# Kernel tuning notes

Hardware: AMD Instinct MI355X
Metric: run time of the kernel (lower is better)

## Reference

```python
import jax, jax.numpy as jnp
import numpy as np

D_MODEL = 1024
NUM_HEADS = 16
D_K = D_MODEL // NUM_HEADS
B, S = 4, 2048
NEG_INF = -1.0e9  # matches torch masked_fill value


def setup_inputs() -> dict:
    key = jax.random.key(0)
    ks = jax.random.split(key, 6)
    scale = 1.0 / np.sqrt(D_MODEL)
    x = jax.random.normal(ks[0], (B, S, D_MODEL), dtype=jnp.float32)
    # causal mask, broadcast over batch and heads: [1,1,S,S]
    mask = jnp.tril(jnp.ones((S, S), dtype=jnp.int32))[None, None]
    Wq = jax.random.normal(ks[1], (D_MODEL, D_MODEL), dtype=jnp.float32) * scale
    Wk = jax.random.normal(ks[2], (D_MODEL, D_MODEL), dtype=jnp.float32) * scale
    Wv = jax.random.normal(ks[3], (D_MODEL, D_MODEL), dtype=jnp.float32) * scale
    Wo = jax.random.normal(ks[4], (D_MODEL, D_MODEL), dtype=jnp.float32) * scale
    bq = jnp.zeros((D_MODEL,), jnp.float32)
    bk = jnp.zeros((D_MODEL,), jnp.float32)
    bv = jnp.zeros((D_MODEL,), jnp.float32)
    bo = jnp.zeros((D_MODEL,), jnp.float32)
    return {"x": x, "mask": mask, "Wq": Wq, "bq": bq, "Wk": Wk, "bk": bk,
            "Wv": Wv, "bv": bv, "Wo": Wo, "bo": bo}


def reference(x, mask, Wq, bq, Wk, bk, Wv, bv, Wo, bo):
    b, s, d = x.shape
    # projections (torch Linear: y = x @ W.T + b)
    q = (x @ Wq.T + bq).reshape(b, s, NUM_HEADS, D_K).transpose(0, 2, 1, 3)  # [B,H,S,Dk]
    k = (x @ Wk.T + bk).reshape(b, s, NUM_HEADS, D_K).transpose(0, 2, 1, 3)
    v = (x @ Wv.T + bv).reshape(b, s, NUM_HEADS, D_K).transpose(0, 2, 1, 3)
    scores = jnp.einsum("bhqd,bhkd->bhqk", q, k) / jnp.sqrt(jnp.float32(D_K))
    scores = jnp.where(mask == 0, NEG_INF, scores)
    attn = jax.nn.softmax(scores, axis=-1)
    out = jnp.einsum("bhqk,bhkd->bhqd", attn, v)  # [B,H,S,Dk]
    out = out.transpose(0, 2, 1, 3).reshape(b, s, d)
    return out @ Wo.T + bo
```

## Files before the change

### kernel.cpp

```cpp
#include <hip/hip_runtime.h>
#include <hip/hip_bf16.h>

#define D_MODEL 1024
#define NUM_HEADS 16
#define DK 64
#define BATCH 4
#define SEQ 2048

typedef __hip_bfloat16 bf16;
typedef __attribute__((ext_vector_type(8))) short bf16x8;
typedef __attribute__((ext_vector_type(4))) short bf16x4;
typedef __attribute__((ext_vector_type(4))) float f32x4;

typedef __attribute__((address_space(1))) const unsigned int gu32;
typedef __attribute__((address_space(3))) unsigned int lu32;

#define QSCALE (0.125f * 1.44269504089f)

__device__ __forceinline__ void gll16(const bf16* g, bf16* l) {
    __builtin_amdgcn_global_load_lds((gu32*)g, (lu32*)l, 16, 0, 0);
}

__device__ __forceinline__ bf16x8 frag_ld(const bf16* lds, int row, int h, int quad) {
    return *(const bf16x8*)(lds + row * 64 + (((h << 2) + quad) ^ (row & 7)) * 8);
}

__global__ __launch_bounds__(256)
void cvt_bf16(const float* __restrict__ x,  const float* __restrict__ Wq,
              const float* __restrict__ Wk, const float* __restrict__ Wv,
              const float* __restrict__ Wo, bf16* __restrict__ xb,
              bf16* __restrict__ Wb)
{
    size_t v = (size_t)blockIdx.x * 256 + threadIdx.x;
    size_t e = v * 4;
    const float* src; bf16* dst; size_t off;
    if (e < 8388608) { src = x; dst = xb; off = e; }
    else {
        size_t r = e - 8388608;
        int w = (int)(r >> 20);
        off = r & 1048575;
        src = (w == 0) ? Wq : (w == 1) ? Wk : (w == 2) ? Wv : Wo;
        dst = Wb + ((size_t)w << 20);
    }
    float4 f = *(const float4*)(src + off);
    bf16 o[4] = {__float2bfloat16(f.x), __float2bfloat16(f.y),
                 __float2bfloat16(f.z), __float2bfloat16(f.w)};
    *(bf16x4*)(dst + off) = *(const bf16x4*)o;
}

template<int MODE>
__global__ __launch_bounds__(512, 2)
void gemm_pipe(const bf16* __restrict__ A, const bf16* __restrict__ W,
               const float* __restrict__ bqv, const float* __restrict__ bkv,
               const float* __restrict__ bvv,
               bf16* __restrict__ Q, bf16* __restrict__ Kt, bf16* __restrict__ Vtr,
               float* __restrict__ fout)
{
    __shared__ bf16 lds[65536];

    const int t = threadIdx.x;
    const int wave = t >> 6, lane = t & 63;
    const int quad = lane >> 4, l16 = lane & 15;
    const int wm = wave >> 2, wn = wave & 3;

    int proj, colb;
    if (MODE == 0) { proj = blockIdx.x >> 2; colb = blockIdx.x & 3; }
    else           { proj = 3;               colb = blockIdx.x;     }
    const int rowBase = blockIdx.y * 256;

    const bf16* Ablk = A + (size_t)rowBase * 1024;
    const bf16* Bblk = W + ((size_t)proj << 20) + (size_t)colb * 256 * 1024;

    auto stage_tile = [&](int d, int k0) {
        bf16* Ad = lds + d * 16384;
        bf16* Bd = lds + 32768 + d * 16384;
        #pragma unroll
        for (int h = 0; h < 2; ++h)
            #pragma unroll
            for (int p = 0; p < 2; ++p) {
                int idx = t + p * 512;
                int row = idx >> 3, cl = idx & 7, cg = cl ^ (row & 7);
                gll16(Ablk + (size_t)(h * 128 + row) * 1024 + k0 + cg * 8,
                      Ad + h * 8192 + idx * 8);
                gll16(Bblk + (size_t)(h * 128 + row) * 1024 + k0 + cg * 8,
                      Bd + h * 8192 + idx * 8);
            }
    };

    f32x4 acc[8][4];
    #pragma unroll
    for (int mf = 0; mf < 8; ++mf)
        #pragma unroll
        for (int nf = 0; nf < 4; ++nf) acc[mf][nf] = (f32x4){0.f, 0.f, 0.f, 0.f};

    auto compute_tile = [&](int d) {
        const bf16* As = lds + d * 16384 + wm * 8192;
        const bf16* Bs = lds + 32768 + d * 16384 + (wn >> 1) * 8192;
        const int brow = (wn & 1) * 64;
        bf16x8 bfr[4][2];
        #pragma unroll
        for (int nf = 0; nf < 4; ++nf) {
            bfr[nf][0] = frag_ld(Bs, brow + nf * 16 + l16, 0, quad);
            bfr[nf][1] = frag_ld(Bs, brow + nf * 16 + l16, 1, quad);
        }
        __builtin_amdgcn_s_setprio(1);
        #pragma unroll
        for (int mf = 0; mf < 8; ++mf) {
            bf16x8 af0 = frag_ld(As, mf * 16 + l16, 0, quad);
            bf16x8 af1 = frag_ld(As, mf * 16 + l16, 1, quad);
            #pragma unroll
            for (int nf = 0; nf < 4; ++nf) {
                acc[mf][nf] = __builtin_amdgcn_mfma_f32_16x16x32_bf16(af0, bfr[nf][0], acc[mf][nf], 0, 0, 0);
                acc[mf][nf] = __builtin_amdgcn_mfma_f32_16x16x32_bf16(af1, bfr[nf][1], acc[mf][nf], 0, 0, 0);
            }
        }
        __builtin_amdgcn_s_setprio(0);
    };

    stage_tile(0, 0);
    stage_tile(1, 64);
    asm volatile("s_waitcnt vmcnt(8)" ::: "memory");
    __builtin_amdgcn_s_barrier();
    asm volatile("" ::: "memory");
    __builtin_amdgcn_sched_barrier(0);

    for (int kt = 0; kt < 16; ++kt) {
        const int d = kt & 1;
        compute_tile(d);

        asm volatile("s_waitcnt lgkmcnt(0)" ::: "memory");
        __builtin_amdgcn_sched_barrier(0);
        __builtin_amdgcn_s_barrier();
        asm volatile("" ::: "memory");

        if (kt + 2 < 16) {
            stage_tile(d, (kt + 2) * 64);
            asm volatile("s_waitcnt vmcnt(8)" ::: "memory");
        } else if (kt + 1 < 16) {
            asm volatile("s_waitcnt vmcnt(0)" ::: "memory");
        }
        if (kt + 1 < 16) {
            __builtin_amdgcn_s_barrier();
            asm volatile("" ::: "memory");
            __builtin_amdgcn_sched_barrier(0);
        }
    }

    if (MODE == 0) {
        const float* bias = proj == 0 ? bqv : (proj == 1 ? bkv : bvv);
        float bias4[4];
        #pragma unroll
        for (int nf = 0; nf < 4; ++nf)
            bias4[nf] = bias[colb * 256 + wn * 64 + nf * 16 + l16];
        const float oscale = proj == 0 ? QSCALE : 1.0f;
        #pragma unroll
        for (int mf = 0; mf < 8; ++mf)
            #pragma unroll
            for (int rr = 0; rr < 4; ++rr) {
                int r = rowBase + wm * 128 + mf * 16 + quad * 4 + rr;
                int b_ = r >> 11, s_ = r & 2047;
                #pragma unroll
                for (int nf = 0; nf < 4; ++nf) {
                    int c = colb * 256 + wn * 64 + nf * 16 + l16;
                    float v = (acc[mf][nf][rr] + bias4[nf]) * oscale;
                    int h_ = c >> 6, d_ = c & 63;
                    size_t bh = (size_t)(b_ * NUM_HEADS + h_);
                    if (proj == 2)
                        Vtr[(bh * DK + d_) * SEQ + s_] = __float2bfloat16(v);
                    else {
                        bf16* dst = proj == 0 ? Q : Kt;
                        dst[(bh * SEQ + s_) * DK + d_] = __float2bfloat16(v);
                    }
                }
            }
    } else {
        #pragma unroll
        for (int mf = 0; mf < 8; ++mf)
            #pragma unroll
            for (int rr = 0; rr < 4; ++rr) {
                int r = rowBase + wm * 128 + mf * 16 + quad * 4 + rr;
                #pragma unroll
                for (int nf = 0; nf < 4; ++nf) {
                    int c = colb * 256 + wn * 64 + nf * 16 + l16;
                    fout[(size_t)r * 1024 + c] = acc[mf][nf][rr] + bqv[c];
                }
            }
    }
}

#define AS 72

__device__ __forceinline__ void stage_attn(const bf16* __restrict__ Kb,
                                           const bf16* __restrict__ Vb,
                                           int k0, bf16* ks, bf16* vs, int t)
{
    #pragma unroll
    for (int p = 0; p < 2; ++p) {
        int idx = t + p * 256;
        int row = idx >> 3, cl = idx & 7;
        int cg = cl ^ (row & 7);
        gll16(Kb + (size_t)(k0 + row) * DK + cg * 8, ks + idx * 8);
        gll16(Vb + (size_t)row * SEQ + k0 + cg * 8, vs + idx * 8);
    }
}

__global__ __launch_bounds__(256)
void attn_mfma(const bf16* __restrict__ Q, const bf16* __restrict__ K,
               const bf16* __restrict__ Vt, bf16* __restrict__ ctx)
{
    __shared__ bf16 Ks[2][64 * 64];
    __shared__ bf16 Vs[2][64 * 64];
    __shared__ bf16 Ps[4][2][16 * AS];

    const int t    = threadIdx.x;
    const int wave = t >> 6, lane = t & 63;
    const int quad = lane >> 4, l16 = lane & 15;
    const int bh   = blockIdx.x;
    const int qbi  = 15 - blockIdx.y;
    const int b_ = bh >> 4, h_ = bh & 15;

    const bf16* Qb = Q  + (size_t)bh * SEQ * DK;
    const bf16* Kb = K  + (size_t)bh * SEQ * DK;
    const bf16* Vb = Vt + (size_t)bh * DK * SEQ;

    const int qb  = qbi * 128;
    const int ntiles = 2 * qbi + 2;

    bf16x8 qf[2][2];
    #pragma unroll
    for (int i = 0; i < 2; ++i) {
        const int qrow = qb + wave * 32 + i * 16 + l16;
        qf[i][0] = *(const bf16x8*)(Qb + (size_t)qrow * DK + quad * 8);
        qf[i][1] = *(const bf16x8*)(Qb + (size_t)qrow * DK + 32 + quad * 8);
    }

    f32x4 O[2][4];
    float lsum[2][4];
    #pragma unroll
    for (int i = 0; i < 2; ++i)
        #pragma unroll
        for (int nc = 0; nc < 4; ++nc) {
            O[i][nc] = (f32x4){0.f, 0.f, 0.f, 0.f};
            lsum[i][nc] = 0.f;
        }

    stage_attn(Kb, Vb, 0, Ks[0], Vs[0], t);
    __syncthreads();

    for (int kt = 0; kt < ntiles; ++kt) {
        const int cur = kt & 1;
        const int k0  = kt * 64;
        if (kt + 1 < ntiles)
            stage_attn(Kb, Vb, k0 + 64, Ks[cur ^ 1], Vs[cur ^ 1], t);

        const bool diag = (kt + 2 >= ntiles);
        const bool skip = (kt == ntiles - 1) && (wave < 2);

        if (!skip) {
            bf16x8 kf[4][2];
            #pragma unroll
            for (int h = 0; h < 4; ++h) {
                kf[h][0] = frag_ld(Ks[cur], h * 16 + l16, 0, quad);
                kf[h][1] = frag_ld(Ks[cur], h * 16 + l16, 1, quad);
            }

            #pragma unroll
            for (int i = 0; i < 2; ++i) {
                const int qrow0i = qb + wave * 32 + i * 16;
                float lacc[4];
                #pragma unroll
                for (int r = 0; r < 4; ++r) lacc[r] = lsum[i][r];
                #pragma unroll
                for (int h = 0; h < 4; ++h) {
                    f32x4 a = (f32x4){0.f, 0.f, 0.f, 0.f};
                    a = __builtin_amdgcn_mfma_f32_16x16x32_bf16(qf[i][0], kf[h][0], a, 0, 0, 0);
                    a = __builtin_amdgcn_mfma_f32_16x16x32_bf16(qf[i][1], kf[h][1], a, 0, 0, 0);
                    #pragma unroll
                    for (int r = 0; r < 4; ++r) {
                        float ss = a[r];
                        if (diag && (k0 + h * 16 + l16 > qrow0i + quad * 4 + r))
                            ss = -1e30f;
                        float p = exp2f(ss);
                        lacc[r] += p;
                        Ps[wave][i][(quad * 4 + r) * AS + h * 16 + l16] =
                            __float2bfloat16(p);
                    }
                }
                #pragma unroll
                for (int r = 0; r < 4; ++r) lsum[i][r] = lacc[r];
            }

            bf16x8 pf[2][2];
            #pragma unroll
            for (int i = 0; i < 2; ++i) {
                pf[i][0] = *(const bf16x8*)(&Ps[wave][i][l16 * AS + quad * 8]);
                pf[i][1] = *(const bf16x8*)(&Ps[wave][i][l16 * AS + 32 + quad * 8]);
            }
            __builtin_amdgcn_s_setprio(1);
            #pragma unroll
            for (int nc = 0; nc < 4; ++nc) {
                bf16x8 vf0 = frag_ld(Vs[cur], nc * 16 + l16, 0, quad);
                bf16x8 vf1 = frag_ld(Vs[cur], nc * 16 + l16, 1, quad);
                #pragma unroll
                for (int i = 0; i < 2; ++i) {
                    O[i][nc] = __builtin_amdgcn_mfma_f32_16x16x32_bf16(pf[i][0], vf0, O[i][nc], 0, 0, 0);
                    O[i][nc] = __builtin_amdgcn_mfma_f32_16x16x32_bf16(pf[i][1], vf1, O[i][nc], 0, 0, 0);
                }
            }
            __builtin_amdgcn_s_setprio(0);
        }
        __syncthreads();
    }

    #pragma unroll
    for (int i = 0; i < 2; ++i) {
        #pragma unroll
        for (int r = 0; r < 4; ++r) {
            #pragma unroll
            for (int off = 1; off < 16; off <<= 1)
                lsum[i][r] += __shfl_xor(lsum[i][r], off, 64);
        }
        #pragma unroll
        for (int nc = 0; nc < 4; ++nc)
            #pragma unroll
            for (int r = 0; r < 4; ++r) {
                const int row = qb + wave * 32 + i * 16 + quad * 4 + r;
                float v = O[i][nc][r] / lsum[i][r];
                ctx[((size_t)(b_ * SEQ + row)) * D_MODEL + h_ * DK + nc * 16 + l16] =
                    __float2bfloat16(v);
            }
    }
}

extern "C" void kernel_launch(void* const* d_in, const int* in_sizes, int n_in,
                              void* d_out, int out_size, void* d_ws, size_t ws_size,
                              hipStream_t stream) {
    const float* x  = (const float*)d_in[0];
    const float* Wq = (const float*)d_in[2];
    const float* bq = (const float*)d_in[3];
    const float* Wk = (const float*)d_in[4];
    const float* bk = (const float*)d_in[5];
    const float* Wv = (const float*)d_in[6];
    const float* bv = (const float*)d_in[7];
    const float* Wo = (const float*)d_in[8];
    const float* bo = (const float*)d_in[9];
    float* out = (float*)d_out;

    const size_t per = (size_t)BATCH * NUM_HEADS * SEQ * DK;
    bf16* Q   = (bf16*)d_ws;
    bf16* Kt  = Q  + per;
    bf16* Vtr = Kt + per;
    bf16* xb  = Vtr + per;
    bf16* ctx = xb;
    bf16* Wb  = xb + per;

    hipLaunchKernelGGL(cvt_bf16, dim3(12288), dim3(256), 0, stream,
                       x, Wq, Wk, Wv, Wo, xb, Wb);

    hipLaunchKernelGGL((gemm_pipe<0>), dim3(12, 32), dim3(512), 0, stream,
                       xb, Wb, bq, bk, bv, Q, Kt, Vtr, (float*)nullptr);

    hipLaunchKernelGGL(attn_mfma, dim3(64, 16), dim3(256), 0,
                       stream, Q, Kt, Vtr, ctx);

    hipLaunchKernelGGL((gemm_pipe<1>), dim3(4, 32), dim3(512), 0, stream,
                       ctx, Wb, bo, (const float*)nullptr, (const float*)nullptr,
                       (bf16*)nullptr, (bf16*)nullptr, (bf16*)nullptr, out);
}
```

Baseline: 312.3 us.

## Shrink GEMM tile to 128x256 with four-phase interleaved LDS reads and staging

The projection GEMM block tile drops from 256x256 to 128x256, which doubles the grid (768 and 256 blocks) and halves the accumulators per wave. The main loop is split into four sub-phases, each pairing LDS fragment reads with MFMA work behind barriers. Global-to-LDS staging for the next K tile is spread across those phases instead of issued all at once. The aim is more blocks to fill the CUs and finer overlap of memory with compute. In exchange it adds more barriers and lowers arithmetic intensity, since A/B data is reused across a smaller tile.

```diff
diff --git a/kernel.cpp b/kernel.cpp
--- a/kernel.cpp
+++ b/kernel.cpp
@@ -16,6 +16,8 @@
 typedef __attribute__((address_space(3))) unsigned int lu32;
 
 #define QSCALE (0.125f * 1.44269504089f)
+
+#define FENCE asm volatile("" ::: "memory")
 
 __device__ __forceinline__ void gll16(const bf16* g, bf16* l) {
     __builtin_amdgcn_global_load_lds((gu32*)g, (lu32*)l, 16, 0, 0);
@@ -49,14 +51,14 @@
 }
 
 template<int MODE>
-__global__ __launch_bounds__(512, 2)
+__global__ __launch_bounds__(512, 1)
 void gemm_pipe(const bf16* __restrict__ A, const bf16* __restrict__ W,
                const float* __restrict__ bqv, const float* __restrict__ bkv,
                const float* __restrict__ bvv,
                bf16* __restrict__ Q, bf16* __restrict__ Kt, bf16* __restrict__ Vtr,
                float* __restrict__ fout)
 {
-    __shared__ bf16 lds[65536];
+    __shared__ bf16 lds[49152];
 
     const int t = threadIdx.x;
     const int wave = t >> 6, lane = t & 63;
@@ -66,83 +68,106 @@
     int proj, colb;
     if (MODE == 0) { proj = blockIdx.x >> 2; colb = blockIdx.x & 3; }
     else           { proj = 3;               colb = blockIdx.x;     }
-    const int rowBase = blockIdx.y * 256;
+    const int rowBase = blockIdx.y * 128;
 
     const bf16* Ablk = A + (size_t)rowBase * 1024;
     const bf16* Bblk = W + ((size_t)proj << 20) + (size_t)colb * 256 * 1024;
 
-    auto stage_tile = [&](int d, int k0) {
-        bf16* Ad = lds + d * 16384;
-        bf16* Bd = lds + 32768 + d * 16384;
-        #pragma unroll
-        for (int h = 0; h < 2; ++h)
-            #pragma unroll
-            for (int p = 0; p < 2; ++p) {
-                int idx = t + p * 512;
-                int row = idx >> 3, cl = idx & 7, cg = cl ^ (row & 7);
-                gll16(Ablk + (size_t)(h * 128 + row) * 1024 + k0 + cg * 8,
-                      Ad + h * 8192 + idx * 8);
-                gll16(Bblk + (size_t)(h * 128 + row) * 1024 + k0 + cg * 8,
-                      Bd + h * 8192 + idx * 8);
-            }
+    auto stageA = [&](int b, int k0) {
+        bf16* dst = lds + b * 8192;
+        #pragma unroll
+        for (int p = 0; p < 2; ++p) {
+            int idx = t + p * 512;
+            int row = idx >> 3, cg = (idx & 7) ^ (row & 7);
+            gll16(Ablk + (size_t)row * 1024 + k0 + cg * 8, dst + idx * 8);
+        }
     };
-
-    f32x4 acc[8][4];
-    #pragma unroll
-    for (int mf = 0; mf < 8; ++mf)
+    auto stageBh = [&](int b, int k0, int h) {
+        bf16* dst = lds + 16384 + b * 16384 + h * 8192;
+        #pragma unroll
+        for (int p = 0; p < 2; ++p) {
+            int idx = t + p * 512;
+            int row = idx >> 3, cg = (idx & 7) ^ (row & 7);
+            gll16(Bblk + (size_t)(h * 128 + row) * 1024 + k0 + cg * 8, dst + idx * 8);
+        }
+    };
+
+    f32x4 acc[4][4];
+    #pragma unroll
+    for (int mf = 0; mf < 4; ++mf)
         #pragma unroll
         for (int nf = 0; nf < 4; ++nf) acc[mf][nf] = (f32x4){0.f, 0.f, 0.f, 0.f};
 
-    auto compute_tile = [&](int d) {
-        const bf16* As = lds + d * 16384 + wm * 8192;
-        const bf16* Bs = lds + 32768 + d * 16384 + (wn >> 1) * 8192;
-        const int brow = (wn & 1) * 64;
-        bf16x8 bfr[4][2];
-        #pragma unroll
-        for (int nf = 0; nf < 4; ++nf) {
-            bfr[nf][0] = frag_ld(Bs, brow + nf * 16 + l16, 0, quad);
-            bfr[nf][1] = frag_ld(Bs, brow + nf * 16 + l16, 1, quad);
-        }
-        __builtin_amdgcn_s_setprio(1);
-        #pragma unroll
-        for (int mf = 0; mf < 8; ++mf) {
-            bf16x8 af0 = frag_ld(As, mf * 16 + l16, 0, quad);
-            bf16x8 af1 = frag_ld(As, mf * 16 + l16, 1, quad);
-            #pragma unroll
-            for (int nf = 0; nf < 4; ++nf) {
-                acc[mf][nf] = __builtin_amdgcn_mfma_f32_16x16x32_bf16(af0, bfr[nf][0], acc[mf][nf], 0, 0, 0);
-                acc[mf][nf] = __builtin_amdgcn_mfma_f32_16x16x32_bf16(af1, bfr[nf][1], acc[mf][nf], 0, 0, 0);
-            }
-        }
-        __builtin_amdgcn_s_setprio(0);
-    };
-
-    stage_tile(0, 0);
-    stage_tile(1, 64);
-    asm volatile("s_waitcnt vmcnt(8)" ::: "memory");
-    __builtin_amdgcn_s_barrier();
-    asm volatile("" ::: "memory");
-    __builtin_amdgcn_sched_barrier(0);
+    stageA(0, 0);  stageBh(0, 0, 0);  stageBh(0, 0, 1);
+    stageA(1, 64); stageBh(1, 64, 0); stageBh(1, 64, 1);
+    asm volatile("s_waitcnt vmcnt(6)" ::: "memory");
+    FENCE; __builtin_amdgcn_s_barrier(); FENCE;
 
     for (int kt = 0; kt < 16; ++kt) {
-        const int d = kt & 1;
-        compute_tile(d);
-
-        asm volatile("s_waitcnt lgkmcnt(0)" ::: "memory");
-        __builtin_amdgcn_sched_barrier(0);
-        __builtin_amdgcn_s_barrier();
-        asm volatile("" ::: "memory");
-
-        if (kt + 2 < 16) {
-            stage_tile(d, (kt + 2) * 64);
-            asm volatile("s_waitcnt vmcnt(8)" ::: "memory");
-        } else if (kt + 1 < 16) {
-            asm volatile("s_waitcnt vmcnt(0)" ::: "memory");
-        }
+        const int b = kt & 1;
+        const bf16* As = lds + b * 8192;
+        const bf16* Bs = lds + 16384 + b * 16384;
+        const int k2 = (kt + 2) * 64;
+        const bool more = (kt + 2) < 16;
+
+        bf16x8 aA[2][2], aB[2][2], bA[2][2], bB[2][2];
+
+        auto rdA = [&](bf16x8 (&f)[2][2], int mh) {
+            #pragma unroll
+            for (int m2 = 0; m2 < 2; ++m2)
+                #pragma unroll
+                for (int kk = 0; kk < 2; ++kk)
+                    f[m2][kk] = frag_ld(As, wm * 64 + (mh * 2 + m2) * 16 + l16, kk, quad);
+        };
+        auto rdB = [&](bf16x8 (&f)[2][2], int nh) {
+            #pragma unroll
+            for (int n2 = 0; n2 < 2; ++n2)
+                #pragma unroll
+                for (int kk = 0; kk < 2; ++kk)
+                    f[n2][kk] = frag_ld(Bs, wn * 64 + (nh * 2 + n2) * 16 + l16, kk, quad);
+        };
+        auto mfma8 = [&](bf16x8 (&af)[2][2], bf16x8 (&bfr)[2][2], int mo, int no) {
+            __builtin_amdgcn_s_setprio(1);
+            #pragma unroll
+            for (int kk = 0; kk < 2; ++kk)
+                #pragma unroll
+                for (int m2 = 0; m2 < 2; ++m2)
+                    #pragma unroll
+                    for (int n2 = 0; n2 < 2; ++n2)
+                        acc[mo + m2][no + n2] = __builtin_amdgcn_mfma_f32_16x16x32_bf16(
+                            af[m2][kk], bfr[n2][kk], acc[mo + m2][no + n2], 0, 0, 0);
+            __builtin_amdgcn_s_setprio(0);
+        };
+        auto bar_open = [] {
+            FENCE; __builtin_amdgcn_s_barrier();
+            asm volatile("s_waitcnt lgkmcnt(0)" ::: "memory");
+            __builtin_amdgcn_sched_barrier(0);
+        };
+        auto bar_close = [] { FENCE; __builtin_amdgcn_s_barrier(); FENCE; };
+
+        rdA(aA, 0); rdB(bA, 0);
+        bar_open();
+        mfma8(aA, bA, 0, 0);
+        bar_close();
+
+        rdB(bB, 1);
+        bar_open();
+        mfma8(aA, bB, 0, 2);
+        bar_close();
+
+        rdA(aB, 1);
+        if (more) stageBh(b, k2, 0);
+        bar_open();
+        mfma8(aB, bB, 2, 2);
+        bar_close();
+
+        if (more) { stageBh(b, k2, 1); stageA(b, k2); }
+        bar_open();
+        mfma8(aB, bA, 2, 0);
         if (kt + 1 < 16) {
-            __builtin_amdgcn_s_barrier();
-            asm volatile("" ::: "memory");
-            __builtin_amdgcn_sched_barrier(0);
+            if (more) asm volatile("s_waitcnt vmcnt(6)" ::: "memory");
+            else      asm volatile("s_waitcnt vmcnt(0)" ::: "memory");
+            bar_close();
         }
     }
 
@@ -154,10 +179,10 @@
             bias4[nf] = bias[colb * 256 + wn * 64 + nf * 16 + l16];
         const float oscale = proj == 0 ? QSCALE : 1.0f;
         #pragma unroll
-        for (int mf = 0; mf < 8; ++mf)
+        for (int mf = 0; mf < 4; ++mf)
             #pragma unroll
             for (int rr = 0; rr < 4; ++rr) {
-                int r = rowBase + wm * 128 + mf * 16 + quad * 4 + rr;
+                int r = rowBase + wm * 64 + mf * 16 + quad * 4 + rr;
                 int b_ = r >> 11, s_ = r & 2047;
                 #pragma unroll
                 for (int nf = 0; nf < 4; ++nf) {
@@ -175,10 +200,10 @@
             }
     } else {
         #pragma unroll
-        for (int mf = 0; mf < 8; ++mf)
+        for (int mf = 0; mf < 4; ++mf)
             #pragma unroll
             for (int rr = 0; rr < 4; ++rr) {
-                int r = rowBase + wm * 128 + mf * 16 + quad * 4 + rr;
+                int r = rowBase + wm * 64 + mf * 16 + quad * 4 + rr;
                 #pragma unroll
                 for (int nf = 0; nf < 4; ++nf) {
                     int c = colb * 256 + wn * 64 + nf * 16 + l16;
@@ -357,13 +382,13 @@
     hipLaunchKernelGGL(cvt_bf16, dim3(12288), dim3(256), 0, stream,
                        x, Wq, Wk, Wv, Wo, xb, Wb);
 
-    hipLaunchKernelGGL((gemm_pipe<0>), dim3(12, 32), dim3(512), 0, stream,
+    hipLaunchKernelGGL((gemm_pipe<0>), dim3(12, 64), dim3(512), 0, stream,
                        xb, Wb, bq, bk, bv, Q, Kt, Vtr, (float*)nullptr);
 
     hipLaunchKernelGGL(attn_mfma, dim3(64, 16), dim3(256), 0,
                        stream, Q, Kt, Vtr, ctx);
 
-    hipLaunchKernelGGL((gemm_pipe<1>), dim3(4, 32), dim3(512), 0, stream,
+    hipLaunchKernelGGL((gemm_pipe<1>), dim3(4, 64), dim3(512), 0, stream,
                        ctx, Wb, bo, (const float*)nullptr, (const float*)nullptr,
                        (bf16*)nullptr, (bf16*)nullptr, (bf16*)nullptr, out);
 }
```

Result: faster. 299.4 us (-4.1%).

## Restructure projection GEMM main loop into ping-pong quarter-tile schedule with interleaved loads

Applied to the files above, without the earlier changes.

The projection GEMM main loop now processes two k-tiles per iteration and splits each into four 64x32 MFMA quadrants. LDS fragment reads and half-tile global-to-LDS prefetches are interleaved between barrier-bracketed MFMA bursts, so memory traffic overlaps compute more finely. Launch bounds drop from two blocks per CU to one, trading occupancy for more registers. Column-block addressing is simplified to a flat index. The added barriers and the dependence on exact vmcnt and lgkmcnt counts raise the risk of stalls or ordering bugs.

```diff
diff --git a/kernel.cpp b/kernel.cpp
--- a/kernel.cpp
+++ b/kernel.cpp
@@ -16,6 +16,12 @@
 typedef __attribute__((address_space(3))) unsigned int lu32;
 
 #define QSCALE (0.125f * 1.44269504089f)
+
+#define FENCE asm volatile("" ::: "memory")
+#define BAR_OPEN()  do { FENCE; __builtin_amdgcn_s_barrier();              \
+    asm volatile("s_waitcnt lgkmcnt(0)" ::: "memory");                     \
+    __builtin_amdgcn_sched_barrier(0); } while (0)
+#define BAR_CLOSE() do { FENCE; __builtin_amdgcn_s_barrier(); FENCE; } while (0)
 
 __device__ __forceinline__ void gll16(const bf16* g, bf16* l) {
     __builtin_amdgcn_global_load_lds((gu32*)g, (lu32*)l, 16, 0, 0);
@@ -49,7 +55,7 @@
 }
 
 template<int MODE>
-__global__ __launch_bounds__(512, 2)
+__global__ __launch_bounds__(512, 1)
 void gemm_pipe(const bf16* __restrict__ A, const bf16* __restrict__ W,
                const float* __restrict__ bqv, const float* __restrict__ bkv,
                const float* __restrict__ bvv,
@@ -63,28 +69,30 @@
     const int quad = lane >> 4, l16 = lane & 15;
     const int wm = wave >> 2, wn = wave & 3;
 
-    int proj, colb;
-    if (MODE == 0) { proj = blockIdx.x >> 2; colb = blockIdx.x & 3; }
-    else           { proj = 3;               colb = blockIdx.x;     }
+    const int colb = blockIdx.x;
     const int rowBase = blockIdx.y * 256;
 
     const bf16* Ablk = A + (size_t)rowBase * 1024;
-    const bf16* Bblk = W + ((size_t)proj << 20) + (size_t)colb * 256 * 1024;
-
-    auto stage_tile = [&](int d, int k0) {
-        bf16* Ad = lds + d * 16384;
-        bf16* Bd = lds + 32768 + d * 16384;
-        #pragma unroll
-        for (int h = 0; h < 2; ++h)
-            #pragma unroll
-            for (int p = 0; p < 2; ++p) {
-                int idx = t + p * 512;
-                int row = idx >> 3, cl = idx & 7, cg = cl ^ (row & 7);
-                gll16(Ablk + (size_t)(h * 128 + row) * 1024 + k0 + cg * 8,
-                      Ad + h * 8192 + idx * 8);
-                gll16(Bblk + (size_t)(h * 128 + row) * 1024 + k0 + cg * 8,
-                      Bd + h * 8192 + idx * 8);
-            }
+    const bf16* Bblk = W + (MODE == 1 ? ((size_t)3 << 20) : (size_t)0)
+                         + (size_t)colb * 256 * 1024;
+
+    auto stageAhalf = [&](int d, int h, int k0) {
+        bf16* dst = (bf16*)lds + d * 16384 + h * 8192;
+        #pragma unroll
+        for (int p = 0; p < 2; ++p) {
+            int idx = t + p * 512;
+            int row = idx >> 3, cg = (idx & 7) ^ (row & 7);
+            gll16(Ablk + (size_t)(h * 128 + row) * 1024 + k0 + cg * 8, dst + idx * 8);
+        }
+    };
+    auto stageBhalf = [&](int d, int h, int k0) {
+        bf16* dst = (bf16*)lds + 32768 + d * 16384 + h * 8192;
+        #pragma unroll
+        for (int p = 0; p < 2; ++p) {
+            int idx = t + p * 512;
+            int row = idx >> 3, cg = (idx & 7) ^ (row & 7);
+            gll16(Bblk + (size_t)(h * 128 + row) * 1024 + k0 + cg * 8, dst + idx * 8);
+        }
     };
 
     f32x4 acc[8][4];
@@ -93,65 +101,99 @@
         #pragma unroll
         for (int nf = 0; nf < 4; ++nf) acc[mf][nf] = (f32x4){0.f, 0.f, 0.f, 0.f};
 
-    auto compute_tile = [&](int d) {
-        const bf16* As = lds + d * 16384 + wm * 8192;
-        const bf16* Bs = lds + 32768 + d * 16384 + (wn >> 1) * 8192;
-        const int brow = (wn & 1) * 64;
-        bf16x8 bfr[4][2];
-        #pragma unroll
-        for (int nf = 0; nf < 4; ++nf) {
-            bfr[nf][0] = frag_ld(Bs, brow + nf * 16 + l16, 0, quad);
-            bfr[nf][1] = frag_ld(Bs, brow + nf * 16 + l16, 1, quad);
-        }
+    const bf16* Aha = (const bf16*)lds + wm * 8192;
+    const bf16* Ahb = (const bf16*)lds + 16384 + wm * 8192;
+    const bf16* Bha = (const bf16*)lds + 32768 + (wn >> 1) * 8192;
+    const bf16* Bhb = (const bf16*)lds + 49152 + (wn >> 1) * 8192;
+    const int brow0 = (wn & 1) * 64;
+
+    auto rdA4 = [&](bf16x8 (&f)[4][2], const bf16* Ah, int mh) {
+        #pragma unroll
+        for (int m4 = 0; m4 < 4; ++m4)
+            #pragma unroll
+            for (int kk = 0; kk < 2; ++kk)
+                f[m4][kk] = frag_ld(Ah, mh * 64 + m4 * 16 + l16, kk, quad);
+    };
+    auto rdB2 = [&](bf16x8 (&f)[2][2], const bf16* Bh, int nh) {
+        #pragma unroll
+        for (int n2 = 0; n2 < 2; ++n2)
+            #pragma unroll
+            for (int kk = 0; kk < 2; ++kk)
+                f[n2][kk] = frag_ld(Bh, brow0 + nh * 32 + n2 * 16 + l16, kk, quad);
+    };
+    auto mfma16 = [&](bf16x8 (&af)[4][2], bf16x8 (&bfr)[2][2], int mh, int nh) {
         __builtin_amdgcn_s_setprio(1);
         #pragma unroll
-        for (int mf = 0; mf < 8; ++mf) {
-            bf16x8 af0 = frag_ld(As, mf * 16 + l16, 0, quad);
-            bf16x8 af1 = frag_ld(As, mf * 16 + l16, 1, quad);
-            #pragma unroll
-            for (int nf = 0; nf < 4; ++nf) {
-                acc[mf][nf] = __builtin_amdgcn_mfma_f32_16x16x32_bf16(af0, bfr[nf][0], acc[mf][nf], 0, 0, 0);
-                acc[mf][nf] = __builtin_amdgcn_mfma_f32_16x16x32_bf16(af1, bfr[nf][1], acc[mf][nf], 0, 0, 0);
-            }
-        }
+        for (int kk = 0; kk < 2; ++kk)
+            #pragma unroll
+            for (int m4 = 0; m4 < 4; ++m4)
+                #pragma unroll
+                for (int n2 = 0; n2 < 2; ++n2)
+                    acc[mh * 4 + m4][nh * 2 + n2] =
+                        __builtin_amdgcn_mfma_f32_16x16x32_bf16(
+                            af[m4][kk], bfr[n2][kk], acc[mh * 4 + m4][nh * 2 + n2],
+                            0, 0, 0);
         __builtin_amdgcn_s_setprio(0);
     };
 
-    stage_tile(0, 0);
-    stage_tile(1, 64);
+    stageBhalf(0, 0, 0);  stageBhalf(0, 1, 0);
+    stageAhalf(0, 0, 0);  stageAhalf(0, 1, 0);
+    stageBhalf(1, 0, 64); stageBhalf(1, 1, 64);
+    stageAhalf(1, 0, 64); stageAhalf(1, 1, 64);
     asm volatile("s_waitcnt vmcnt(8)" ::: "memory");
-    __builtin_amdgcn_s_barrier();
-    asm volatile("" ::: "memory");
-    __builtin_amdgcn_sched_barrier(0);
-
-    for (int kt = 0; kt < 16; ++kt) {
-        const int d = kt & 1;
-        compute_tile(d);
-
-        asm volatile("s_waitcnt lgkmcnt(0)" ::: "memory");
-        __builtin_amdgcn_sched_barrier(0);
-        __builtin_amdgcn_s_barrier();
-        asm volatile("" ::: "memory");
-
-        if (kt + 2 < 16) {
-            stage_tile(d, (kt + 2) * 64);
+    FENCE; __builtin_amdgcn_s_barrier(); FENCE;
+
+    for (int it = 0; it < 8; ++it) {
+        const bool more = (it < 7);
+        const int ka2 = it * 128 + 128, kb2 = ka2 + 64;
+        bf16x8 aX[4][2], aY[4][2], bX[2][2], bY[2][2];
+
+        rdA4(aX, Aha, 0); rdB2(bX, Bha, 0);
+        asm volatile("s_waitcnt lgkmcnt(8)" ::: "memory");
+        BAR_OPEN(); mfma16(aX, bX, 0, 0); BAR_CLOSE();
+
+        rdB2(bY, Bha, 1);
+        BAR_OPEN(); mfma16(aX, bY, 0, 1); BAR_CLOSE();
+
+        rdA4(aY, Aha, 1);
+        if (more) stageBhalf(0, 0, ka2);
+        BAR_OPEN(); mfma16(aY, bY, 1, 1); BAR_CLOSE();
+
+        if (more) stageBhalf(0, 1, ka2);
+        BAR_OPEN(); mfma16(aY, bX, 1, 0);
+        if (more) asm volatile("s_waitcnt vmcnt(4)" ::: "memory");
+        else      asm volatile("s_waitcnt vmcnt(0)" ::: "memory");
+        BAR_CLOSE();
+
+        rdA4(aX, Ahb, 0); rdB2(bX, Bhb, 0);
+        if (more) stageAhalf(0, 0, ka2);
+        asm volatile("s_waitcnt lgkmcnt(8)" ::: "memory");
+        BAR_OPEN(); mfma16(aX, bX, 0, 0); BAR_CLOSE();
+
+        rdB2(bY, Bhb, 1);
+        if (more) stageAhalf(0, 1, ka2);
+        BAR_OPEN(); mfma16(aX, bY, 0, 1); BAR_CLOSE();
+
+        rdA4(aY, Ahb, 1);
+        if (more) { stageBhalf(1, 0, kb2); stageBhalf(1, 1, kb2); }
+        BAR_OPEN(); mfma16(aY, bY, 1, 1); BAR_CLOSE();
+
+        if (more) { stageAhalf(1, 0, kb2); stageAhalf(1, 1, kb2); }
+        BAR_OPEN(); mfma16(aY, bX, 1, 0);
+        if (more) {
             asm volatile("s_waitcnt vmcnt(8)" ::: "memory");
-        } else if (kt + 1 < 16) {
-            asm volatile("s_waitcnt vmcnt(0)" ::: "memory");
-        }
-        if (kt + 1 < 16) {
-            __builtin_amdgcn_s_barrier();
-            asm volatile("" ::: "memory");
-            __builtin_amdgcn_sched_barrier(0);
+            BAR_CLOSE();
         }
     }
 
     if (MODE == 0) {
+        const int proj = colb >> 2;
         const float* bias = proj == 0 ? bqv : (proj == 1 ? bkv : bvv);
+        const int cb = (colb & 3) * 256;
         float bias4[4];
         #pragma unroll
         for (int nf = 0; nf < 4; ++nf)
-            bias4[nf] = bias[colb * 256 + wn * 64 + nf * 16 + l16];
+            bias4[nf] = bias[cb + wn * 64 + nf * 16 + l16];
         const float oscale = proj == 0 ? QSCALE : 1.0f;
         #pragma unroll
         for (int mf = 0; mf < 8; ++mf)
@@ -161,7 +203,7 @@
                 int b_ = r >> 11, s_ = r & 2047;
                 #pragma unroll
                 for (int nf = 0; nf < 4; ++nf) {
-                    int c = colb * 256 + wn * 64 + nf * 16 + l16;
+                    int c = cb + wn * 64 + nf * 16 + l16;
                     float v = (acc[mf][nf][rr] + bias4[nf]) * oscale;
                     int h_ = c >> 6, d_ = c & 63;
                     size_t bh = (size_t)(b_ * NUM_HEADS + h_);
```

Result: faster. 304.8 us (-2.4%).
